# Kernel optimization log

Measured on AMD Instinct MI355X. Metric: run time of the kernel, lower is better.

The kernel has to match this reference:

```python
import jax, jax.numpy as jnp
import numpy as np

B, H, L, V = 128, 1024, 60, 50257


def setup_inputs() -> dict:
    key = jax.random.key(0)
    ks = jax.random.split(key, 14)
    s = 0.02
    f32 = jnp.float32
    return {
        "input": jax.random.randint(ks[0], (B,), 0, V),
        "hidden": jax.random.normal(ks[1], (1, B, H), f32),
        "encoder_outputs": jax.random.normal(ks[2], (B, L, H), f32),
        # learned parameters
        "emb": (jax.random.normal(ks[3], (V, H), f32) * s),
        "attn_W": (jax.random.normal(ks[4], (L, 2 * H), f32) * s),
        "attn_b": jnp.zeros((L,), f32),
        "comb_W": (jax.random.normal(ks[5], (H, 2 * H), f32) * s),
        "comb_b": jnp.zeros((H,), f32),
        "W_ih": (jax.random.normal(ks[6], (3 * H, H), f32) * s),
        "W_hh": (jax.random.normal(ks[7], (3 * H, H), f32) * s),
        "b_ih": jnp.zeros((3 * H,), f32),
        "b_hh": jnp.zeros((3 * H,), f32),
        "out_W": (jax.random.normal(ks[8], (V, H), f32) * s),
        "out_b": jnp.zeros((V,), f32),
    }


def reference(input, hidden, encoder_outputs, emb, attn_W, attn_b,
              comb_W, comb_b, W_ih, W_hh, b_ih, b_hh, out_W, out_b):
    # embedding lookup (dropout is identity in eval mode)
    embedded = emb[input]                      # [B, H]
    h = hidden[0]                              # [B, H]

    # Bahdanau-style attention over fixed max_length positions
    attn_logits = jnp.concatenate([embedded, h], axis=1) @ attn_W.T + attn_b  # [B, L]
    attn_weights = jax.nn.softmax(attn_logits, axis=1)                        # [B, L]
    attn_applied = jnp.einsum('bl,blh->bh', attn_weights, encoder_outputs)    # [B, H]

    # combine + relu
    x = jnp.concatenate([embedded, attn_applied], axis=1) @ comb_W.T + comb_b  # [B, H]
    x = jax.nn.relu(x)

    # single GRU step (PyTorch gate order: r, z, n)
    gi = x @ W_ih.T + b_ih                     # [B, 3H]
    gh = h @ W_hh.T + b_hh                     # [B, 3H]
    i_r, i_z, i_n = jnp.split(gi, 3, axis=1)
    h_r, h_z, h_n = jnp.split(gh, 3, axis=1)
    r = jax.nn.sigmoid(i_r + h_r)
    z = jax.nn.sigmoid(i_z + h_z)
    n = jnp.tanh(i_n + r * h_n)
    h_new = (1.0 - z) * n + z * h              # [B, H]

    # output projection + log_softmax over vocab
    logp = jax.nn.log_softmax(h_new @ out_W.T + out_b, axis=1)  # [B, V]
    return logp, h_new[None], attn_weights
```

## Files before the change

### kernel.cpp

```cpp
#include <hip/hip_runtime.h>
#include <hip/hip_bf16.h>

#define B_ 128
#define H_ 1024
#define L_ 60
#define V_ 50257
#define NPB_ 786
#define NMP_ (NPB_ * 4)

typedef __attribute__((ext_vector_type(8))) short bf16x8;
typedef __attribute__((ext_vector_type(4))) short bf16x4;
typedef __attribute__((ext_vector_type(4))) float f32x4;

__device__ __forceinline__ unsigned short f2bf(float f) {
  union { __hip_bfloat16 h; unsigned short u; } v;
  v.h = __float2bfloat16(f);
  return v.u;
}

__device__ __forceinline__ bf16x8 cvt8(float4 a, float4 b) {
  union { bf16x8 v; __hip_bfloat16 h[8]; } u;
  u.h[0] = __float2bfloat16(a.x); u.h[1] = __float2bfloat16(a.y);
  u.h[2] = __float2bfloat16(a.z); u.h[3] = __float2bfloat16(a.w);
  u.h[4] = __float2bfloat16(b.x); u.h[5] = __float2bfloat16(b.y);
  u.h[6] = __float2bfloat16(b.z); u.h[7] = __float2bfloat16(b.w);
  return u.v;
}

__device__ __forceinline__ bf16x4 cvt4(float4 a) {
  bf16x4 v;
  v[0] = (short)f2bf(a.x); v[1] = (short)f2bf(a.y);
  v[2] = (short)f2bf(a.z); v[3] = (short)f2bf(a.w);
  return v;
}

#define SBAR()   __builtin_amdgcn_s_barrier()
#define SCHED0() __builtin_amdgcn_sched_barrier(0)
__device__ __forceinline__ void lwait0() { asm volatile("s_waitcnt lgkmcnt(0)" ::: "memory"); }

__device__ __forceinline__ size_t packIdx(int b, int k) {
  int s = k >> 5;
  int bm = b >> 4;
  int lane = (b & 15) | (((k >> 3) & 3) << 4);
  return ((size_t)((s * 8 + bm) * 64 + lane) << 3) | (size_t)(k & 7);
}

__global__ __launch_bounds__(256) void k_front(
    const int* __restrict__ input, const float* __restrict__ hidden,
    const float* __restrict__ emb, const float* __restrict__ attn_W,
    const float* __restrict__ attn_b, unsigned short* __restrict__ aXa,
    unsigned short* __restrict__ aH, float* __restrict__ lbuf)
{
  int bx = blockIdx.x;
  if (bx < 512) {
    int idx = bx * 256 + threadIdx.x;
    int b = idx >> 10, j = idx & (H_ - 1);
    float e = emb[(size_t)input[b] * H_ + j];
    float h = hidden[idx];
    size_t p = packIdx(b, j);
    aXa[p] = f2bf(e);
    aH[p]  = f2bf(h);
  } else {
    int t = threadIdx.x, wv = t >> 6, lane = t & 63;
    int task = (bx - 512) * 4 + wv;
    int b = task / L_, l = task - b * L_;
    const float* erow = emb + (size_t)input[b] * H_;
    const float* hrow = hidden + (size_t)b * H_;
    const float* wr = attn_W + (size_t)l * (2 * H_);
    float acc = 0.f;
    #pragma unroll 4
    for (int i = 0; i < 16; ++i) {
      int m = lane + i * 64;
      acc += erow[m] * wr[m] + hrow[m] * wr[H_ + m];
    }
    #pragma unroll
    for (int off = 32; off; off >>= 1) acc += __shfl_xor(acc, off);
    if (lane == 0) lbuf[b * 64 + l] = acc + attn_b[l];
  }
}

__global__ __launch_bounds__(256) void k_appsm(
    const float* __restrict__ enc, const float* __restrict__ lbuf,
    float* __restrict__ attnw, unsigned short* __restrict__ aXa)
{
  __shared__ float sWt[64];
  int b = blockIdx.x, q = blockIdx.y, t = threadIdx.x;
  if (t < 64) {
    float v = (t < L_) ? lbuf[b * 64 + t] : -1e30f;
    float m = v;
    #pragma unroll
    for (int off = 32; off; off >>= 1) m = fmaxf(m, __shfl_xor(m, off));
    float e = (t < L_) ? __expf(v - m) : 0.f;
    float s = e;
    #pragma unroll
    for (int off = 32; off; off >>= 1) s += __shfl_xor(s, off);
    float w = e / s;
    sWt[t] = w;
    if (q == 0 && t < L_) attnw[b * L_ + t] = w;
  }
  __syncthreads();
  int col = q * 256 + t;
  const float* eb = enc + (size_t)b * L_ * H_ + col;
  float acc = 0.f;
  #pragma unroll 4
  for (int l = 0; l < L_; ++l) acc += sWt[l] * eb[(size_t)l * H_];
  aXa[packIdx(b, H_ + col)] = f2bf(acc);
}

__global__ __launch_bounds__(256, 4) void k_gemm(
    const unsigned short* __restrict__ Apk, const unsigned short* __restrict__ Apk2,
    const float* __restrict__ Wt, const float* __restrict__ Wt2,
    float* __restrict__ Cpart, float* __restrict__ Cpart2,
    int K, int N, int nchunks, int halfY)
{
  __shared__ __align__(16) unsigned short bufW0[64 * 32];
  __shared__ __align__(16) unsigned short bufW1[64 * 32];
  int t = threadIdx.x, wv = t >> 6, lane = t & 63;
  int y = blockIdx.y;
  const unsigned short* A = Apk;
  const float* W = Wt;
  float* CP = Cpart;
  int sidx = y;
  if (halfY && y >= halfY) { A = Apk2; W = Wt2; CP = Cpart2; sidx = y - halfY; }
  int chunk0 = sidx * nchunks;
  int n0 = blockIdx.x * 64;
  int ch = wv & 1;
  int bm0 = (wv >> 1) * 4;
  int g = lane >> 4;

  int sr  = wv * 16 + (lane >> 2);
  int sj  = lane & 3;
  int ssl = sj ^ ((sr >> 1) & 3);
  int sgcol = n0 + sr; sgcol = (sgcol < N) ? sgcol : (N - 1);
  const float* wsrc = W + (size_t)sgcol * K + sj * 8;
  unsigned short* wdst0 = &bufW0[sr * 32 + ssl * 8];
  unsigned short* wdst1 = &bufW1[sr * 32 + ssl * 8];

  f32x4 acc[4][2];
  #pragma unroll
  for (int i = 0; i < 4; ++i)
    #pragma unroll
    for (int j = 0; j < 2; ++j) acc[i][j] = (f32x4){0.f, 0.f, 0.f, 0.f};

  auto GW = [&](int kc, float4& lo, float4& hi) {
    const float* p = wsrc + (size_t)kc * 32;
    lo = *(const float4*)p;
    hi = *(const float4*)(p + 4);
  };
  const bf16x8* apg = (const bf16x8*)A;
  auto LA = [&](int kc, bf16x8* x) {
    #pragma unroll
    for (int j = 0; j < 4; ++j)
      x[j] = apg[((size_t)kc * 8 + bm0 + j) * 64 + lane];
  };
  auto COMP = [&](const unsigned short* buf, const bf16x8* a) {
    #pragma unroll
    for (int nci = 0; nci < 2; ++nci) {
      int rr = (ch * 2 + nci) * 16 + (lane & 15);
      int s = g ^ ((rr >> 1) & 3);
      bf16x8 bfr = *(const bf16x8*)&buf[rr * 32 + s * 8];
      #pragma unroll
      for (int j = 0; j < 4; ++j)
        acc[j][nci] = __builtin_amdgcn_mfma_f32_16x16x32_bf16(a[j], bfr, acc[j][nci], 0, 0, 0);
    }
  };

  float4 lo0, hi0, lo1, hi1;
  bf16x8 aA[4], aB[4];
  GW(chunk0, lo0, hi0); LA(chunk0, aA);

  for (int kk = 0; kk < nchunks; kk += 2) {
    if (kk + 1 < nchunks) { GW(chunk0 + kk + 1, lo1, hi1); LA(chunk0 + kk + 1, aB); }
    *(bf16x8*)wdst0 = cvt8(lo0, hi0);
    lwait0(); SCHED0(); SBAR(); SCHED0();
    COMP(bufW0, aA);
    if (kk + 1 >= nchunks) break;
    if (kk + 2 < nchunks) { GW(chunk0 + kk + 2, lo0, hi0); LA(chunk0 + kk + 2, aA); }
    *(bf16x8*)wdst1 = cvt8(lo1, hi1);
    lwait0(); SCHED0(); SBAR(); SCHED0();
    COMP(bufW1, aB);
  }

  float* dst = CP + (size_t)sidx * B_ * N;
  int rb = (lane >> 4) * 4;
  #pragma unroll
  for (int bm = 0; bm < 4; ++bm)
    #pragma unroll
    for (int r = 0; r < 4; ++r) {
      int row = (bm0 + bm) * 16 + rb + r;
      #pragma unroll
      for (int nci = 0; nci < 2; ++nci) {
        int c = n0 + (ch * 2 + nci) * 16 + (lane & 15);
        if (c < N) dst[(size_t)row * N + c] = acc[bm][nci][r];
      }
    }
}

__global__ __launch_bounds__(512, 4) void k_proj(
    const unsigned short* __restrict__ Apk, const float* __restrict__ W,
    const float* __restrict__ bias, float* __restrict__ logits,
    float* __restrict__ pms)
{
  __shared__ __align__(16) unsigned short bufW[2][64 * 256];
  int t = threadIdx.x, w = t >> 6, lane = t & 63;
  int n0 = blockIdx.x * 64;
  int mh = w >> 2, cg = w & 3;
  int bm0 = mh * 4;

  int srow0 = w * 8;
  const bf16x8* apg = (const bf16x8*)Apk;

  f32x4 acc[4];
  #pragma unroll
  for (int i = 0; i < 4; ++i) acc[i] = (f32x4){0.f, 0.f, 0.f, 0.f};

  auto LD = [&](int c, float4* rg) {
    #pragma unroll
    for (int i = 0; i < 8; ++i) {
      int rr = srow0 + i;
      int gr = n0 + rr; gr = (gr < V_) ? gr : (V_ - 1);
      rg[i] = *(const float4*)(W + (size_t)gr * H_ + c * 256 + lane * 4);
    }
  };
  auto WR = [&](int bi, const float4* rg) {
    #pragma unroll
    for (int i = 0; i < 8; ++i) {
      int rr = srow0 + i;
      int off = rr * 256 + (((lane >> 1) ^ (rr & 7)) << 3) + ((lane & 1) << 2);
      *(bf16x4*)&bufW[bi][off] = cvt4(rg[i]);
    }
  };
  auto COMP = [&](int bi, int c) {
    int rr = cg * 16 + (lane & 15);
    #pragma unroll
    for (int ks = 0; ks < 8; ++ks) {
      int phys = ((ks << 2) + (lane >> 4)) ^ (lane & 7);
      bf16x8 bw = *(const bf16x8*)&bufW[bi][rr * 256 + (phys << 3)];
      int s = c * 8 + ks;
      #pragma unroll
      for (int bm = 0; bm < 4; ++bm) {
        bf16x8 af = apg[((size_t)s * 8 + bm0 + bm) * 64 + lane];
        acc[bm] = __builtin_amdgcn_mfma_f32_16x16x32_bf16(af, bw, acc[bm], 0, 0, 0);
      }
    }
  };

  float4 rA[8], rB[8];
  LD(0, rA);
  LD(1, rB);
  WR(0, rA);
  lwait0(); SCHED0(); SBAR(); SCHED0();
  LD(2, rA);
  COMP(0, 0);
  WR(1, rB);
  lwait0(); SCHED0(); SBAR(); SCHED0();
  LD(3, rB);
  COMP(1, 1);
  WR(0, rA);
  lwait0(); SCHED0(); SBAR(); SCHED0();
  COMP(0, 2);
  WR(1, rB);
  lwait0(); SCHED0(); SBAR(); SCHED0();
  COMP(1, 3);

  int col = n0 + cg * 16 + (lane & 15);
  float bv = (col < V_) ? bias[col] : 0.f;
  int rb = (lane >> 4) * 4;
  #pragma unroll
  for (int bm = 0; bm < 4; ++bm)
    #pragma unroll
    for (int r = 0; r < 4; ++r) {
      int row = mh * 64 + bm * 16 + rb + r;
      float v = acc[bm][r] + bv;
      if (col < V_) logits[(size_t)row * V_ + col] = v;
      float m = (col < V_) ? v : -1e30f;
      #pragma unroll
      for (int off = 8; off; off >>= 1) m = fmaxf(m, __shfl_xor(m, off));
      float e = (col < V_) ? __expf(v - m) : 0.f;
      #pragma unroll
      for (int off = 8; off; off >>= 1) e += __shfl_xor(e, off);
      if ((lane & 15) == 0) {
        size_t o = ((size_t)row * NMP_ + blockIdx.x * 4 + cg) * 2;
        pms[o] = m; pms[o + 1] = e;
      }
    }
}

__global__ __launch_bounds__(256) void k_reduce_comb(
    const float* __restrict__ parts, const float* __restrict__ bias,
    unsigned short* __restrict__ aX)
{
  int idx = blockIdx.x * 256 + threadIdx.x;
  int b = idx >> 10, j = idx & (H_ - 1);
  float s = bias[j];
  #pragma unroll
  for (int p = 0; p < 16; ++p) s += parts[(size_t)p * B_ * H_ + idx];
  s = fmaxf(s, 0.f);
  aX[packIdx(b, j)] = f2bf(s);
}

__global__ __launch_bounds__(256) void k_gate(
    const float* __restrict__ giP, const float* __restrict__ ghP,
    const float* __restrict__ b_ih, const float* __restrict__ b_hh,
    const float* __restrict__ hidden, float* __restrict__ hnew,
    unsigned short* __restrict__ aHn)
{
  int idx = blockIdx.x * 256 + threadIdx.x;
  int b = idx >> 10, j = idx & (H_ - 1);
  size_t base = (size_t)b * 3 * H_;
  float ir = b_ih[j], iz = b_ih[H_ + j], in_ = b_ih[2 * H_ + j];
  float hr = b_hh[j], hz = b_hh[H_ + j], hn = b_hh[2 * H_ + j];
  #pragma unroll
  for (int p = 0; p < 4; ++p) {
    const float* gi = giP + (size_t)p * B_ * 3 * H_ + base;
    const float* gh = ghP + (size_t)p * B_ * 3 * H_ + base;
    ir += gi[j]; iz += gi[H_ + j]; in_ += gi[2 * H_ + j];
    hr += gh[j]; hz += gh[H_ + j]; hn += gh[2 * H_ + j];
  }
  float r = 1.f / (1.f + __expf(-(ir + hr)));
  float z = 1.f / (1.f + __expf(-(iz + hz)));
  float n = tanhf(in_ + r * hn);
  float h = hidden[idx];
  float hv = (1.f - z) * n + z * h;
  hnew[idx] = hv;
  aHn[packIdx(b, j)] = f2bf(hv);
}

#define SL_ 6283
__global__ __launch_bounds__(256) void k_lsub(
    float* __restrict__ logits, const float* __restrict__ pms, int nblk2)
{
  __shared__ float sm[4], ss[4], sc;
  int b = blockIdx.x, sl = blockIdx.y, t = threadIdx.x;
  float M = -1e30f, S = 0.f;
  for (int i = t; i < nblk2; i += 256) {
    float m = pms[((size_t)b * nblk2 + i) * 2];
    float s = pms[((size_t)b * nblk2 + i) * 2 + 1];
    float nm = fmaxf(M, m);
    S = S * __expf(M - nm) + s * __expf(m - nm);
    M = nm;
  }
  #pragma unroll
  for (int off = 32; off; off >>= 1) {
    float m2 = __shfl_xor(M, off), s2 = __shfl_xor(S, off);
    float nm = fmaxf(M, m2);
    S = S * __expf(M - nm) + s2 * __expf(m2 - nm);
    M = nm;
  }
  if ((t & 63) == 0) { sm[t >> 6] = M; ss[t >> 6] = S; }
  __syncthreads();
  if (t == 0) {
    float Mf = sm[0], Sf = ss[0];
    #pragma unroll
    for (int i = 1; i < 4; ++i) {
      float nm = fmaxf(Mf, sm[i]);
      Sf = Sf * __expf(Mf - nm) + ss[i] * __expf(sm[i] - nm);
      Mf = nm;
    }
    sc = Mf + logf(Sf);
  }
  __syncthreads();
  float c = sc;
  int v0 = sl * SL_;
  int v1 = v0 + SL_; if (v1 > V_) v1 = V_;
  float* row = logits + (size_t)b * V_;
  for (int v = v0 + t; v < v1; v += 256) row[v] -= c;
}

extern "C" void kernel_launch(void* const* d_in, const int* in_sizes, int n_in,
                              void* d_out, int out_size, void* d_ws, size_t ws_size,
                              hipStream_t stream)
{
  const int*   input  = (const int*)d_in[0];
  const float* hidden = (const float*)d_in[1];
  const float* enc    = (const float*)d_in[2];
  const float* emb    = (const float*)d_in[3];
  const float* attn_W = (const float*)d_in[4];
  const float* attn_b = (const float*)d_in[5];
  const float* comb_W = (const float*)d_in[6];
  const float* comb_b = (const float*)d_in[7];
  const float* W_ih   = (const float*)d_in[8];
  const float* W_hh   = (const float*)d_in[9];
  const float* b_ih   = (const float*)d_in[10];
  const float* b_hh   = (const float*)d_in[11];
  const float* out_W  = (const float*)d_in[12];
  const float* out_b  = (const float*)d_in[13];

  float* out    = (float*)d_out;
  float* logits = out;
  float* hnew   = out + (size_t)B_ * V_;
  float* attnw  = hnew + (size_t)B_ * H_;

  char* ws = (char*)d_ws;
  unsigned short* aXa = (unsigned short*)(ws);
  unsigned short* aH  = (unsigned short*)(ws + 524288);
  unsigned short* aX  = (unsigned short*)(ws + 786432);
  unsigned short* aHn = (unsigned short*)(ws + 1048576);
  float* lbuf  = (float*)(ws + 1310720);
  float* pms   = (float*)(ws + 1343488);
  float* combP = (float*)(ws + 4587520);
  float* giP   = (float*)(ws + 4587520);
  float* ghP   = (float*)(ws + 4587520 + 6291456);

  k_front<<<512 + (B_ * L_) / 4, 256, 0, stream>>>(input, hidden, emb, attn_W, attn_b,
                                                   aXa, aH, lbuf);
  k_appsm<<<dim3(B_, 4), 256, 0, stream>>>(enc, lbuf, attnw, aXa);
  k_gemm<<<dim3(16, 16), 256, 0, stream>>>(aXa, nullptr, comb_W, nullptr,
                                           combP, nullptr, 2 * H_, H_, 4, 0);
  k_reduce_comb<<<(B_ * H_) / 256, 256, 0, stream>>>(combP, comb_b, aX);
  k_gemm<<<dim3(48, 8), 256, 0, stream>>>(aX, aH, W_ih, W_hh,
                                          giP, ghP, H_, 3 * H_, 8, 4);
  k_gate<<<(B_ * H_) / 256, 256, 0, stream>>>(giP, ghP, b_ih, b_hh, hidden, hnew, aHn);
  k_proj<<<NPB_, 512, 0, stream>>>(aHn, out_W, out_b, logits, pms);
  k_lsub<<<dim3(B_, 8), 256, 0, stream>>>(logits, pms, NMP_);
}
```

Before: 157.2 us.

## Rewrite output projection to stream fp32 weights via direct global-to-LDS loads

The vocab projection kernel now uses 256-thread blocks where each wave owns 16 output columns over all 128 batch rows. It streams fp32 weight slices straight into per-wave LDS with global_load_lds, double-buffered on vmcnt waits, and converts to bf16 only when reading fragments. Block indices are remapped so each XCD gets a contiguous range of column tiles. The aim is to take the register staging and block-wide barriers off the dominant weight-streaming path and improve L2 locality. The cost is small 32-wide K steps with more MFMA issue overhead and A-fragment reloads every step.

```diff
diff --git a/kernel.cpp b/kernel.cpp
--- a/kernel.cpp
+++ b/kernel.cpp
@@ -9,7 +9,6 @@
 #define NMP_ (NPB_ * 4)
 
 typedef __attribute__((ext_vector_type(8))) short bf16x8;
-typedef __attribute__((ext_vector_type(4))) short bf16x4;
 typedef __attribute__((ext_vector_type(4))) float f32x4;
 
 __device__ __forceinline__ unsigned short f2bf(float f) {
@@ -27,16 +26,17 @@
   return u.v;
 }
 
-__device__ __forceinline__ bf16x4 cvt4(float4 a) {
-  bf16x4 v;
-  v[0] = (short)f2bf(a.x); v[1] = (short)f2bf(a.y);
-  v[2] = (short)f2bf(a.z); v[3] = (short)f2bf(a.w);
-  return v;
+__device__ __forceinline__ void gl_lds16(const void* g, void* l) {
+  __builtin_amdgcn_global_load_lds(
+      (const __attribute__((address_space(1))) unsigned int*)g,
+      (__attribute__((address_space(3))) unsigned int*)l, 16, 0, 0);
 }
 
 #define SBAR()   __builtin_amdgcn_s_barrier()
 #define SCHED0() __builtin_amdgcn_sched_barrier(0)
 __device__ __forceinline__ void lwait0() { asm volatile("s_waitcnt lgkmcnt(0)" ::: "memory"); }
+__device__ __forceinline__ void vwait2() { asm volatile("s_waitcnt vmcnt(2)" ::: "memory"); }
+__device__ __forceinline__ void vwait0() { asm volatile("s_waitcnt vmcnt(0)" ::: "memory"); }
 
 __device__ __forceinline__ size_t packIdx(int b, int k) {
   int s = k >> 5;
@@ -196,81 +196,77 @@
     }
 }
 
-__global__ __launch_bounds__(512, 4) void k_proj(
+__global__ __launch_bounds__(256, 6) void k_proj(
     const unsigned short* __restrict__ Apk, const float* __restrict__ W,
     const float* __restrict__ bias, float* __restrict__ logits,
     float* __restrict__ pms)
 {
-  __shared__ __align__(16) unsigned short bufW[2][64 * 256];
+  __shared__ __align__(16) float lds[4][2][512];
   int t = threadIdx.x, w = t >> 6, lane = t & 63;
-  int n0 = blockIdx.x * 64;
-  int mh = w >> 2, cg = w & 3;
-  int bm0 = mh * 4;
-
-  int srow0 = w * 8;
+  int bid = blockIdx.x;
+  int qq8 = NPB_ / 8, r8 = NPB_ % 8;
+  int xcd = bid & 7, sub = bid >> 3;
+  int blk = (xcd < r8 ? xcd * (qq8 + 1) : r8 * (qq8 + 1) + (xcd - r8) * qq8) + sub;
+  int n0 = blk * 64;
+  int cg = w;
+  int srow = lane >> 3, sg = lane & 7;
+  int rr = lane & 15, qg = lane >> 4;
+  int pp = (qg ^ ((rr >> 1) & 3)) * 8;
+
   const bf16x8* apg = (const bf16x8*)Apk;
 
-  f32x4 acc[4];
-  #pragma unroll
-  for (int i = 0; i < 4; ++i) acc[i] = (f32x4){0.f, 0.f, 0.f, 0.f};
-
-  auto LD = [&](int c, float4* rg) {
-    #pragma unroll
-    for (int i = 0; i < 8; ++i) {
-      int rr = srow0 + i;
-      int gr = n0 + rr; gr = (gr < V_) ? gr : (V_ - 1);
-      rg[i] = *(const float4*)(W + (size_t)gr * H_ + c * 256 + lane * 4);
-    }
-  };
-  auto WR = [&](int bi, const float4* rg) {
-    #pragma unroll
-    for (int i = 0; i < 8; ++i) {
-      int rr = srow0 + i;
-      int off = rr * 256 + (((lane >> 1) ^ (rr & 7)) << 3) + ((lane & 1) << 2);
-      *(bf16x4*)&bufW[bi][off] = cvt4(rg[i]);
-    }
-  };
-  auto COMP = [&](int bi, int c) {
-    int rr = cg * 16 + (lane & 15);
-    #pragma unroll
-    for (int ks = 0; ks < 8; ++ks) {
-      int phys = ((ks << 2) + (lane >> 4)) ^ (lane & 7);
-      bf16x8 bw = *(const bf16x8*)&bufW[bi][rr * 256 + (phys << 3)];
-      int s = c * 8 + ks;
-      #pragma unroll
-      for (int bm = 0; bm < 4; ++bm) {
-        bf16x8 af = apg[((size_t)s * 8 + bm0 + bm) * 64 + lane];
-        acc[bm] = __builtin_amdgcn_mfma_f32_16x16x32_bf16(af, bw, acc[bm], 0, 0, 0);
-      }
-    }
-  };
-
-  float4 rA[8], rB[8];
-  LD(0, rA);
-  LD(1, rB);
-  WR(0, rA);
-  lwait0(); SCHED0(); SBAR(); SCHED0();
-  LD(2, rA);
-  COMP(0, 0);
-  WR(1, rB);
-  lwait0(); SCHED0(); SBAR(); SCHED0();
-  LD(3, rB);
-  COMP(1, 1);
-  WR(0, rA);
-  lwait0(); SCHED0(); SBAR(); SCHED0();
-  COMP(0, 2);
-  WR(1, rB);
-  lwait0(); SCHED0(); SBAR(); SCHED0();
-  COMP(1, 3);
-
-  int col = n0 + cg * 16 + (lane & 15);
+  f32x4 acc[8];
+  #pragma unroll
+  for (int i = 0; i < 8; ++i) acc[i] = (f32x4){0.f, 0.f, 0.f, 0.f};
+
+  auto STAGE = [&](int kc, int buf) {
+    #pragma unroll
+    for (int i = 0; i < 2; ++i) {
+      int rw = i * 8 + srow;
+      int col = n0 + cg * 16 + rw; if (col >= V_) col = V_ - 1;
+      int gs = sg ^ (rw & 6);
+      const float* src = W + (size_t)col * H_ + kc * 32 + gs * 4;
+      gl_lds16(src, &lds[w][buf][i * 256]);
+    }
+  };
+  bf16x8 aA[8];
+  auto LA = [&](int kc) {
+    #pragma unroll
+    for (int bm = 0; bm < 8; ++bm)
+      aA[bm] = apg[((size_t)kc * 8 + bm) * 64 + lane];
+  };
+  auto COMP = [&](int buf) {
+    const float* bw = &lds[w][buf][0];
+    float4 lo = *(const float4*)&bw[rr * 32 + pp];
+    float4 hi = *(const float4*)&bw[rr * 32 + pp + 4];
+    bf16x8 bfr = cvt8(lo, hi);
+    #pragma unroll
+    for (int bm = 0; bm < 8; ++bm)
+      acc[bm] = __builtin_amdgcn_mfma_f32_16x16x32_bf16(aA[bm], bfr, acc[bm], 0, 0, 0);
+  };
+
+  STAGE(0, 0);
+  for (int c = 0; c < 32; c += 2) {
+    LA(c);
+    if (c + 1 < 32) STAGE(c + 1, 1);
+    vwait2(); SCHED0();
+    COMP(0);
+    SCHED0();
+    LA(c + 1);
+    if (c + 2 < 32) STAGE(c + 2, 0);
+    if (c + 2 < 32) vwait2(); else vwait0();
+    SCHED0();
+    COMP(1);
+    SCHED0();
+  }
+
+  int col = n0 + cg * 16 + rr;
   float bv = (col < V_) ? bias[col] : 0.f;
-  int rb = (lane >> 4) * 4;
-  #pragma unroll
-  for (int bm = 0; bm < 4; ++bm)
+  #pragma unroll
+  for (int bm = 0; bm < 8; ++bm)
     #pragma unroll
     for (int r = 0; r < 4; ++r) {
-      int row = mh * 64 + bm * 16 + rb + r;
+      int row = bm * 16 + qg * 4 + r;
       float v = acc[bm][r] + bv;
       if (col < V_) logits[(size_t)row * V_ + col] = v;
       float m = (col < V_) ? v : -1e30f;
@@ -279,8 +275,8 @@
       float e = (col < V_) ? __expf(v - m) : 0.f;
       #pragma unroll
       for (int off = 8; off; off >>= 1) e += __shfl_xor(e, off);
-      if ((lane & 15) == 0) {
-        size_t o = ((size_t)row * NMP_ + blockIdx.x * 4 + cg) * 2;
+      if (rr == 0) {
+        size_t o = ((size_t)row * NMP_ + blk * 4 + cg) * 2;
         pms[o] = m; pms[o + 1] = e;
       }
     }
@@ -411,6 +407,6 @@
   k_gemm<<<dim3(48, 8), 256, 0, stream>>>(aX, aH, W_ih, W_hh,
                                           giP, ghP, H_, 3 * H_, 8, 4);
   k_gate<<<(B_ * H_) / 256, 256, 0, stream>>>(giP, ghP, b_ih, b_hh, hidden, hnew, aHn);
-  k_proj<<<NPB_, 512, 0, stream>>>(aHn, out_W, out_b, logits, pms);
+  k_proj<<<NPB_, 256, 0, stream>>>(aHn, out_W, out_b, logits, pms);
   k_lsub<<<dim3(B_, 8), 256, 0, stream>>>(logits, pms, NMP_);
 }
```

Result: slower. 221.4 us (+40.9%).
